# Optimization experiments

Hardware: AMD Instinct MI355X
Metric: run time of the kernel (lower is better)

Reference implementation:

```python
import jax, jax.numpy as jnp
import numpy as np

N, M = 30000, 32
VX, VY, VZ = 0.2, 0.2, 4.0
XOFF, YOFF, ZOFF = 0.1, -39.9, -1.0  # vx/2+pc_range[0], vy/2+pc_range[1], vz/2+pc_range[2]
EPS = 1e-3
H = 3  # num_heads, head_dim = 3 // 3 = 1


def setup_inputs() -> dict:
    key = jax.random.key(0)
    ks = jax.random.split(key, 13)
    features = jax.random.normal(ks[0], (N, M, 4), jnp.float32)
    num_points = jax.random.randint(ks[1], (N,), 1, M + 1, dtype=jnp.int32)
    coors = jax.random.randint(ks[2], (N, 4), 0, 352, dtype=jnp.int32)
    # PFN layer params (Linear 10->64 no bias, BN1d affine)
    pfn_w = jax.random.normal(ks[3], (10, 64), jnp.float32) * 0.1
    bn_gamma = jnp.ones((64,), jnp.float32)
    bn_beta = jnp.zeros((64,), jnp.float32)
    # PillarAttention: MHA on 3-dim coords, 3 heads of dim 1
    wq = jax.random.normal(ks[4], (3, 3), jnp.float32) * 0.5
    wk = jax.random.normal(ks[5], (3, 3), jnp.float32) * 0.5
    wv = jax.random.normal(ks[6], (3, 3), jnp.float32) * 0.5
    wo = jax.random.normal(ks[7], (3, 3), jnp.float32) * 0.5
    bq = jax.random.normal(ks[8], (3,), jnp.float32) * 0.02
    bk = jax.random.normal(ks[9], (3,), jnp.float32) * 0.02
    bv = jax.random.normal(ks[10], (3,), jnp.float32) * 0.02
    bo = jax.random.normal(ks[11], (3,), jnp.float32) * 0.02
    return dict(features=features, num_points=num_points, coors=coors,
                pfn_w=pfn_w, bn_gamma=bn_gamma, bn_beta=bn_beta,
                wq=wq, wk=wk, wv=wv, wo=wo, bq=bq, bk=bk, bv=bv, bo=bo)


def _pillar_attention(xyz, wq, wk, wv, wo, bq, bk, bv, bo):
    # xyz: (N, M, 3); 3 heads of dim 1 -> per-head score is an outer product
    q = xyz @ wq + bq  # (N, M, 3)
    k = xyz @ wk + bk
    v = xyz @ wv + bv
    # head_dim = 1 => scale = 1/sqrt(1) = 1
    scores = jnp.einsum('nih,njh->nhij', q, k)          # (N, H, M, M)
    attn = jax.nn.softmax(scores, axis=-1)
    out = jnp.einsum('nhij,njh->nih', attn, v)          # (N, M, 3)
    return out @ wo + bo


def reference(features, num_points, coors, pfn_w, bn_gamma, bn_beta,
              wq, wk, wv, wo, bq, bk, bv, bo):
    dtype = features.dtype
    xyz = features[:, :, :3]  # original coords (attn & cluster use these, pre in-place write)

    # PillarAttention on raw xyz, then max over feature dim
    feat_attn = _pillar_attention(xyz, wq, wk, wv, wo, bq, bk, bv, bo)  # (N, M, 3)
    max_attn = jnp.max(feat_attn, axis=-1, keepdims=True)              # (N, M, 1)

    npts = num_points.astype(dtype)[:, None, None]                      # (N,1,1)
    # cluster center offsets (uses original xyz)
    points_mean = jnp.sum(xyz, axis=1, keepdims=True) / npts
    f_cluster = xyz - points_mean                                       # (N, M, 3)

    # voxel center offsets; coors = [batch, z, y, x]
    cf = coors.astype(dtype)
    cx = cf[:, 3] * VX + XOFF
    cy = cf[:, 2] * VY + YOFF
    cz = cf[:, 1] * VZ + ZOFF
    f_center = jnp.stack([xyz[:, :, 0] - cx[:, None],
                          xyz[:, :, 1] - cy[:, None],
                          xyz[:, :, 2] - cz[:, None]], axis=-1)          # (N, M, 3)

    # legacy=True in-place bug: features[:, :, :3] becomes f_center before concat
    feats = jnp.concatenate([f_center, features[:, :, 3:], f_cluster, f_center], axis=-1)  # (N, M, 10)

    # mask out padded points
    mask = (jnp.arange(M)[None, :] < num_points[:, None]).astype(dtype)[:, :, None]
    feats = feats * mask

    # PFNLayer (last_vfe=True): Linear -> BN1d (train-mode stats over N*M) -> LeakyReLU
    x = feats @ pfn_w                                                    # (N, M, 64)
    mean = jnp.mean(x, axis=(0, 1))
    var = jnp.var(x, axis=(0, 1))
    x = (x - mean) * jax.lax.rsqrt(var + EPS) * bn_gamma + bn_beta
    x = jax.nn.leaky_relu(x, negative_slope=0.01)                        # (N, M, 64)

    # attention-weighted max pool fused with plain max pool
    fa = max_attn * x / jnp.sum(max_attn, axis=1, keepdims=True)
    fa = jnp.max(fa, axis=1, keepdims=True)                              # (N, 1, 64)
    fm = jnp.max(x, axis=1, keepdims=True)                               # (N, 1, 64)
    f = (fa + fm) * 0.5
    return f[:, 0, :]                                                    # (N, 64)
```

## Files before the change

### kernel.cpp

```cpp
#include <hip/hip_runtime.h>
#include <float.h>
#include <math.h>

constexpr int NP = 30000;
constexpr int M  = 32;
constexpr float VXc = 0.2f, VYc = 0.2f, VZc = 4.0f;
constexpr float XOFFc = 0.1f, YOFFc = -39.9f, ZOFFc = -1.0f;

typedef __attribute__((ext_vector_type(8)))  short bf16x8;
typedef __attribute__((ext_vector_type(16))) float f32x16;

__device__ __forceinline__ unsigned short f2bf(float x) {
    unsigned int u = __builtin_bit_cast(unsigned int, x);
    u = (u + 0x7fffu + ((u >> 16) & 1u)) >> 16;
    return (unsigned short)u;
}

__global__ __launch_bounds__(256) void stats_kernel(
    const float4* __restrict__ fp,
    const int*    __restrict__ num_points,
    const int*    __restrict__ coors,
    float*        __restrict__ Sp)
{
    float S[35];
#pragma unroll
    for (int k = 0; k < 35; ++k) S[k] = 0.f;

    const int stride = gridDim.x * blockDim.x;

    for (int p = blockIdx.x * blockDim.x + threadIdx.x; p < NP * M; p += stride) {
        const int n = p >> 5;
        const int i = p & 31;
        const float4 f = fp[p];

        float sx = f.x, sy = f.y, sz = f.z;
#pragma unroll
        for (int m = 16; m >= 1; m >>= 1) {
            sx += __shfl_xor(sx, m, 32);
            sy += __shfl_xor(sy, m, 32);
            sz += __shfl_xor(sz, m, 32);
        }
        const int npts = num_points[n];
        const float inv = __builtin_amdgcn_rcpf((float)npts);
        const int c1 = coors[4 * n + 1], c2 = coors[4 * n + 2], c3 = coors[4 * n + 3];
        const float cx = (float)c3 * VXc + XOFFc;
        const float cy = (float)c2 * VYc + YOFFc;
        const float cz = (float)c1 * VZc + ZOFFc;
        const bool valid = (i < npts);

        float u[7];
        u[0] = valid ? f.x - cx : 0.f;
        u[1] = valid ? f.y - cy : 0.f;
        u[2] = valid ? f.z - cz : 0.f;
        u[3] = valid ? f.w      : 0.f;
        u[4] = valid ? f.x - sx * inv : 0.f;
        u[5] = valid ? f.y - sy * inv : 0.f;
        u[6] = valid ? f.z - sz * inv : 0.f;

#pragma unroll
        for (int k = 0; k < 7; ++k) S[k] += u[k];
        int idx = 7;
#pragma unroll
        for (int k = 0; k < 7; ++k)
#pragma unroll
            for (int l = k; l < 7; ++l)
                S[idx++] += u[k] * u[l];
    }

#pragma unroll
    for (int k = 0; k < 35; ++k) {
#pragma unroll
        for (int m = 32; m >= 1; m >>= 1) S[k] += __shfl_xor(S[k], m, 64);
    }

    __shared__ float part[4][35];
    const int wid = threadIdx.x >> 6, ln = threadIdx.x & 63;
    if (ln == 0) {
#pragma unroll
        for (int k = 0; k < 35; ++k) part[wid][k] = S[k];
    }
    __syncthreads();
    if (threadIdx.x < 35) {
        Sp[blockIdx.x * 35 + threadIdx.x] =
            part[0][threadIdx.x] + part[1][threadIdx.x] +
            part[2][threadIdx.x] + part[3][threadIdx.x];
    }
}

__global__ __launch_bounds__(320) void affine_kernel(
    const float* __restrict__ Sp,
    int nsb,
    const float* __restrict__ pfn_w,
    const float* __restrict__ gamma,
    const float* __restrict__ beta,
    float*       __restrict__ AB,
    unsigned short* __restrict__ Wpk)
{
    __shared__ double sh[8][36];
    __shared__ double Sd[35];
    const int tid = threadIdx.x;

    if (tid < 280) {
        const int k = tid % 35;
        const int c = tid / 35;
        double acc = 0.0;
        for (int b = c; b < nsb; b += 8)
            acc += (double)Sp[b * 35 + k];
        sh[c][k] = acc;
    }
    __syncthreads();
    if (tid < 35) {
        double a = 0.0;
#pragma unroll
        for (int c = 0; c < 8; ++c) a += sh[c][tid];
        Sd[tid] = a;
    }
    __syncthreads();

    if (tid < 64) {
        const int c = tid;
        double w7[7];
        w7[0] = (double)pfn_w[0 * 64 + c] + (double)pfn_w[7 * 64 + c];
        w7[1] = (double)pfn_w[1 * 64 + c] + (double)pfn_w[8 * 64 + c];
        w7[2] = (double)pfn_w[2 * 64 + c] + (double)pfn_w[9 * 64 + c];
        w7[3] = (double)pfn_w[3 * 64 + c];
        w7[4] = (double)pfn_w[4 * 64 + c];
        w7[5] = (double)pfn_w[5 * 64 + c];
        w7[6] = (double)pfn_w[6 * 64 + c];

        const double invNM = 1.0 / ((double)NP * (double)M);
        double mean = 0.0;
#pragma unroll
        for (int k = 0; k < 7; ++k) mean += Sd[k] * w7[k];
        mean *= invNM;

        double ex2 = 0.0;
        int idx = 7;
#pragma unroll
        for (int k = 0; k < 7; ++k)
#pragma unroll
            for (int l = k; l < 7; ++l) {
                double t = Sd[idx++] * w7[k] * w7[l];
                ex2 += (k == l) ? t : 2.0 * t;
            }
        ex2 *= invNM;

        double var = ex2 - mean * mean;
        double a = (double)gamma[c] / sqrt(var + 1e-3);
        AB[c]      = (float)a;
        AB[64 + c] = (float)((double)beta[c] - mean * a);
    }

    if (tid < 256) {
        const int s = tid;
        const int v = s >> 7;
        const int t = (s >> 6) & 1;
        const int l = s & 63;
        const int half = l >> 5;
        const int n = (l & 31) + 32 * t;
        unsigned short val[8] = {0, 0, 0, 0, 0, 0, 0, 0};
        if (half == v) {
            float w7[7];
            w7[0] = pfn_w[0 * 64 + n] + pfn_w[7 * 64 + n];
            w7[1] = pfn_w[1 * 64 + n] + pfn_w[8 * 64 + n];
            w7[2] = pfn_w[2 * 64 + n] + pfn_w[9 * 64 + n];
            w7[3] = pfn_w[3 * 64 + n];
            w7[4] = pfn_w[4 * 64 + n];
            w7[5] = pfn_w[5 * 64 + n];
            w7[6] = pfn_w[6 * 64 + n];
#pragma unroll
            for (int j = 0; j < 7; ++j) val[j] = f2bf(w7[j]);
        }
#pragma unroll
        for (int j = 0; j < 8; ++j) Wpk[s * 8 + j] = val[j];
    }
}

__global__ __launch_bounds__(256) void main_kernel(
    const float4* __restrict__ fp,
    const int*    __restrict__ num_points,
    const int*    __restrict__ coors,
    const float*  __restrict__ AB,
    const unsigned short* __restrict__ Wpk,
    const float*  __restrict__ wq, const float* __restrict__ wk,
    const float*  __restrict__ wv, const float* __restrict__ wo,
    const float*  __restrict__ bq, const float* __restrict__ bk,
    const float*  __restrict__ bv, const float* __restrict__ bo,
    float*        __restrict__ out)
{
    const int tid  = threadIdx.x;
    const int wave = tid >> 6;
    const int lane = tid & 63;
    const int half = lane >> 5;
    const int i    = lane & 31;
    const int p    = wave * 2 + half;
    const int n    = blockIdx.x * 8 + p;

    __shared__ float kv_s[8][32][8];
    __shared__ float r_s[8][32];

    const float4 f = fp[(size_t)n * M + i];
    const int npts = num_points[n];
    const int c1 = coors[4 * n + 1], c2 = coors[4 * n + 2], c3 = coors[4 * n + 3];
    const float a_t0 = AB[i], a_t1 = AB[32 + i];
    const float b_t0 = AB[64 + i], b_t1 = AB[96 + i];
    const bf16x8 bfA0 = *reinterpret_cast<const bf16x8*>(Wpk + (size_t)(  0 + lane) * 8);
    const bf16x8 bfA1 = *reinterpret_cast<const bf16x8*>(Wpk + (size_t)( 64 + lane) * 8);
    const bf16x8 bfB0 = *reinterpret_cast<const bf16x8*>(Wpk + (size_t)(128 + lane) * 8);
    const bf16x8 bfB1 = *reinterpret_cast<const bf16x8*>(Wpk + (size_t)(192 + lane) * 8);

    float q[3], kk[3], vv[3];
#pragma unroll
    for (int h = 0; h < 3; ++h) {
        q[h]  = f.x * wq[0 * 3 + h] + f.y * wq[1 * 3 + h] + f.z * wq[2 * 3 + h] + bq[h];
        kk[h] = f.x * wk[0 * 3 + h] + f.y * wk[1 * 3 + h] + f.z * wk[2 * 3 + h] + bk[h];
        vv[h] = f.x * wv[0 * 3 + h] + f.y * wv[1 * 3 + h] + f.z * wv[2 * 3 + h] + bv[h];
    }
    *reinterpret_cast<float4*>(&kv_s[p][i][0]) = make_float4(kk[0], vv[0], kk[1], vv[1]);
    *reinterpret_cast<float2*>(&kv_s[p][i][4]) = make_float2(kk[2], vv[2]);

    float sx = f.x, sy = f.y, sz = f.z;
    float kmx[3], kmn[3];
#pragma unroll
    for (int h = 0; h < 3; ++h) { kmx[h] = kk[h]; kmn[h] = kk[h]; }
#pragma unroll
    for (int m = 16; m >= 1; m >>= 1) {
        sx += __shfl_xor(sx, m, 32);
        sy += __shfl_xor(sy, m, 32);
        sz += __shfl_xor(sz, m, 32);
#pragma unroll
        for (int h = 0; h < 3; ++h) {
            kmx[h] = fmaxf(kmx[h], __shfl_xor(kmx[h], m, 32));
            kmn[h] = fminf(kmn[h], __shfl_xor(kmn[h], m, 32));
        }
    }
    __syncthreads();

    const float LOG2E = 1.4426950408889634f;
    float qh2[3], mrow[3];
#pragma unroll
    for (int h = 0; h < 3; ++h) {
        qh2[h]  = q[h] * LOG2E;
        mrow[h] = qh2[h] * (q[h] >= 0.f ? kmx[h] : kmn[h]);
    }
    float den[3] = {0.f, 0.f, 0.f}, num[3] = {0.f, 0.f, 0.f};
#pragma unroll
    for (int j = 0; j < 32; ++j) {
        const float4 kv01 = *reinterpret_cast<const float4*>(&kv_s[p][j][0]);
        const float2 kv2  = *reinterpret_cast<const float2*>(&kv_s[p][j][4]);
        float e0 = __builtin_amdgcn_exp2f(__builtin_fmaf(qh2[0], kv01.x, -mrow[0]));
        float e1 = __builtin_amdgcn_exp2f(__builtin_fmaf(qh2[1], kv01.z, -mrow[1]));
        float e2 = __builtin_amdgcn_exp2f(__builtin_fmaf(qh2[2], kv2.x,  -mrow[2]));
        den[0] += e0; num[0] = __builtin_fmaf(e0, kv01.y, num[0]);
        den[1] += e1; num[1] = __builtin_fmaf(e1, kv01.w, num[1]);
        den[2] += e2; num[2] = __builtin_fmaf(e2, kv2.y,  num[2]);
    }
    const float o0 = num[0] * __builtin_amdgcn_rcpf(den[0]);
    const float o1 = num[1] * __builtin_amdgcn_rcpf(den[1]);
    const float o2 = num[2] * __builtin_amdgcn_rcpf(den[2]);

    float fa0 = o0 * wo[0] + o1 * wo[3] + o2 * wo[6] + bo[0];
    float fa1 = o0 * wo[1] + o1 * wo[4] + o2 * wo[7] + bo[1];
    float fa2 = o0 * wo[2] + o1 * wo[5] + o2 * wo[8] + bo[2];
    float ma  = fmaxf(fa0, fmaxf(fa1, fa2));

    float sum_ma = ma;
#pragma unroll
    for (int m = 16; m >= 1; m >>= 1) sum_ma += __shfl_xor(sum_ma, m, 32);
    r_s[p][i] = ma * __builtin_amdgcn_rcpf(sum_ma);

    const float inv = __builtin_amdgcn_rcpf((float)npts);
    const float cx = (float)c3 * VXc + XOFFc;
    const float cy = (float)c2 * VYc + YOFFc;
    const float cz = (float)c1 * VZc + ZOFFc;
    const bool valid = (i < npts);

    float u[7];
    u[0] = valid ? f.x - cx : 0.f;
    u[1] = valid ? f.y - cy : 0.f;
    u[2] = valid ? f.z - cz : 0.f;
    u[3] = valid ? f.w      : 0.f;
    u[4] = valid ? f.x - sx * inv : 0.f;
    u[5] = valid ? f.y - sy * inv : 0.f;
    u[6] = valid ? f.z - sz * inv : 0.f;

    unsigned int w32[4];
    w32[0] = (unsigned int)f2bf(u[0]) | ((unsigned int)f2bf(u[1]) << 16);
    w32[1] = (unsigned int)f2bf(u[2]) | ((unsigned int)f2bf(u[3]) << 16);
    w32[2] = (unsigned int)f2bf(u[4]) | ((unsigned int)f2bf(u[5]) << 16);
    w32[3] = (unsigned int)f2bf(u[6]);

    union { unsigned int w[4]; bf16x8 v; } ua, ub;
#pragma unroll
    for (int e = 0; e < 4; ++e) {
        ua.w[e] = (half == 0) ? w32[e] : 0u;
        ub.w[e] = (half == 1) ? w32[e] : 0u;
    }

    f32x16 accA0, accA1, accB0, accB1;
#pragma unroll
    for (int e = 0; e < 16; ++e) { accA0[e] = 0.f; accA1[e] = 0.f; accB0[e] = 0.f; accB1[e] = 0.f; }
    accA0 = __builtin_amdgcn_mfma_f32_32x32x16_bf16(ua.v, bfA0, accA0, 0, 0, 0);
    accA1 = __builtin_amdgcn_mfma_f32_32x32x16_bf16(ua.v, bfA1, accA1, 0, 0, 0);
    accB0 = __builtin_amdgcn_mfma_f32_32x32x16_bf16(ub.v, bfB0, accB0, 0, 0, 0);
    accB1 = __builtin_amdgcn_mfma_f32_32x32x16_bf16(ub.v, bfB1, accB1, 0, 0, 0);

    __syncthreads();

    const int pA = wave * 2;
    const int nA = blockIdx.x * 8 + pA;

    {
        float4 rg4[4];
#pragma unroll
        for (int g = 0; g < 4; ++g)
            rg4[g] = *reinterpret_cast<const float4*>(&r_s[pA][g * 8 + 4 * half]);

        float fm0 = -FLT_MAX, fv0 = -FLT_MAX, fm1 = -FLT_MAX, fv1 = -FLT_MAX;
#pragma unroll
        for (int rg = 0; rg < 16; ++rg) {
            const float rr = rg4[rg >> 2][rg & 3];
            float y0 = __builtin_fmaf(accA0[rg], a_t0, b_t0);
            y0 = fmaxf(y0, 0.01f * y0);
            fm0 = fmaxf(fm0, y0); fv0 = fmaxf(fv0, rr * y0);
            float y1 = __builtin_fmaf(accA1[rg], a_t1, b_t1);
            y1 = fmaxf(y1, 0.01f * y1);
            fm1 = fmaxf(fm1, y1); fv1 = fmaxf(fv1, rr * y1);
        }
        fm0 = fmaxf(fm0, __shfl_xor(fm0, 32, 64));
        fv0 = fmaxf(fv0, __shfl_xor(fv0, 32, 64));
        fm1 = fmaxf(fm1, __shfl_xor(fm1, 32, 64));
        fv1 = fmaxf(fv1, __shfl_xor(fv1, 32, 64));
        const float res = (half == 0) ? 0.5f * (fv0 + fm0) : 0.5f * (fv1 + fm1);
        out[(size_t)nA * 64 + 32 * half + i] = res;
    }

    {
        const int pB = pA + 1;
        const int nB = nA + 1;
        float4 rg4[4];
#pragma unroll
        for (int g = 0; g < 4; ++g)
            rg4[g] = *reinterpret_cast<const float4*>(&r_s[pB][g * 8 + 4 * half]);

        float fm0 = -FLT_MAX, fv0 = -FLT_MAX, fm1 = -FLT_MAX, fv1 = -FLT_MAX;
#pragma unroll
        for (int rg = 0; rg < 16; ++rg) {
            const float rr = rg4[rg >> 2][rg & 3];
            float y0 = __builtin_fmaf(accB0[rg], a_t0, b_t0);
            y0 = fmaxf(y0, 0.01f * y0);
            fm0 = fmaxf(fm0, y0); fv0 = fmaxf(fv0, rr * y0);
            float y1 = __builtin_fmaf(accB1[rg], a_t1, b_t1);
            y1 = fmaxf(y1, 0.01f * y1);
            fm1 = fmaxf(fm1, y1); fv1 = fmaxf(fv1, rr * y1);
        }
        fm0 = fmaxf(fm0, __shfl_xor(fm0, 32, 64));
        fv0 = fmaxf(fv0, __shfl_xor(fv0, 32, 64));
        fm1 = fmaxf(fm1, __shfl_xor(fm1, 32, 64));
        fv1 = fmaxf(fv1, __shfl_xor(fv1, 32, 64));
        const float res = (half == 0) ? 0.5f * (fv0 + fm0) : 0.5f * (fv1 + fm1);
        out[(size_t)nB * 64 + 32 * half + i] = res;
    }
}

extern "C" void kernel_launch(void* const* d_in, const int* in_sizes, int n_in,
                              void* d_out, int out_size, void* d_ws, size_t ws_size,
                              hipStream_t stream) {
    const float4* feats  = (const float4*)d_in[0];
    const int*    npts   = (const int*)d_in[1];
    const int*    coors  = (const int*)d_in[2];
    const float*  pfn_w  = (const float*)d_in[3];
    const float*  gamma  = (const float*)d_in[4];
    const float*  beta   = (const float*)d_in[5];
    const float*  wq     = (const float*)d_in[6];
    const float*  wk     = (const float*)d_in[7];
    const float*  wv     = (const float*)d_in[8];
    const float*  wo     = (const float*)d_in[9];
    const float*  bq     = (const float*)d_in[10];
    const float*  bk     = (const float*)d_in[11];
    const float*  bv     = (const float*)d_in[12];
    const float*  bo     = (const float*)d_in[13];
    float*        out    = (float*)d_out;

    int nsb = 480;
    if (ws_size > 0 && ws_size < (size_t)(480 * 140 + 8192)) {
        size_t avail = ws_size > 8192 ? ws_size - 8192 : 140;
        int fit = (int)(avail / 140);
        nsb = fit < 1 ? 1 : (fit > 480 ? 480 : fit);
    }
    size_t ab_off  = ((size_t)(nsb * 140) + 255) & ~(size_t)255;
    float*          Sp  = (float*)d_ws;
    float*          AB  = (float*)((char*)d_ws + ab_off);
    unsigned short* Wpk = (unsigned short*)((char*)d_ws + ab_off + 512);

    stats_kernel<<<nsb, 256, 0, stream>>>(feats, npts, coors, Sp);
    affine_kernel<<<1, 320, 0, stream>>>(Sp, nsb, pfn_w, gamma, beta, AB, Wpk);
    main_kernel<<<NP / 8, 256, 0, stream>>>(feats, npts, coors, AB, Wpk,
                                            wq, wk, wv, wo, bq, bk, bv, bo, out);
}
```

Measured before the change: 154.8 us.

## Fold BN affine into bf16 weights and run one-wave blocks with prefetch loop

The BatchNorm scale is folded into the packed bf16 PFN weights, and the shift rides along as an eighth weight row paired with a constant 1.0 input. That removes the per-element affine FMA and the AB loads in the main kernel. The main kernel now uses 64-thread blocks that loop over four pillar pairs, prefetching the next pair's inputs while computing the current one. The trade is more bf16 rounding on the scaled weights and bias, and less parallelism per block (3750 one-wave blocks).

```diff
diff --git a/kernel.cpp b/kernel.cpp
--- a/kernel.cpp
+++ b/kernel.cpp
@@ -93,11 +93,11 @@
     const float* __restrict__ pfn_w,
     const float* __restrict__ gamma,
     const float* __restrict__ beta,
-    float*       __restrict__ AB,
     unsigned short* __restrict__ Wpk)
 {
     __shared__ double sh[8][36];
     __shared__ double Sd[35];
+    __shared__ float a_sh[64], b_sh[64];
     const int tid = threadIdx.x;
 
     if (tid < 280) {
@@ -147,9 +147,10 @@
 
         double var = ex2 - mean * mean;
         double a = (double)gamma[c] / sqrt(var + 1e-3);
-        AB[c]      = (float)a;
-        AB[64 + c] = (float)((double)beta[c] - mean * a);
-    }
+        a_sh[c] = (float)a;
+        b_sh[c] = (float)((double)beta[c] - mean * a);
+    }
+    __syncthreads();
 
     if (tid < 256) {
         const int s = tid;
@@ -160,6 +161,7 @@
         const int n = (l & 31) + 32 * t;
         unsigned short val[8] = {0, 0, 0, 0, 0, 0, 0, 0};
         if (half == v) {
+            const float a = a_sh[n];
             float w7[7];
             w7[0] = pfn_w[0 * 64 + n] + pfn_w[7 * 64 + n];
             w7[1] = pfn_w[1 * 64 + n] + pfn_w[8 * 64 + n];
@@ -169,18 +171,18 @@
             w7[5] = pfn_w[5 * 64 + n];
             w7[6] = pfn_w[6 * 64 + n];
 #pragma unroll
-            for (int j = 0; j < 7; ++j) val[j] = f2bf(w7[j]);
+            for (int j = 0; j < 7; ++j) val[j] = f2bf(w7[j] * a);
+            val[7] = f2bf(b_sh[n]);
         }
 #pragma unroll
         for (int j = 0; j < 8; ++j) Wpk[s * 8 + j] = val[j];
     }
 }
 
-__global__ __launch_bounds__(256) void main_kernel(
+__global__ __launch_bounds__(64) void main_kernel(
     const float4* __restrict__ fp,
     const int*    __restrict__ num_points,
     const int*    __restrict__ coors,
-    const float*  __restrict__ AB,
     const unsigned short* __restrict__ Wpk,
     const float*  __restrict__ wq, const float* __restrict__ wk,
     const float*  __restrict__ wv, const float* __restrict__ wo,
@@ -188,178 +190,187 @@
     const float*  __restrict__ bv, const float* __restrict__ bo,
     float*        __restrict__ out)
 {
-    const int tid  = threadIdx.x;
-    const int wave = tid >> 6;
-    const int lane = tid & 63;
+    const int lane = threadIdx.x;
     const int half = lane >> 5;
     const int i    = lane & 31;
-    const int p    = wave * 2 + half;
-    const int n    = blockIdx.x * 8 + p;
-
-    __shared__ float kv_s[8][32][8];
-    __shared__ float r_s[8][32];
-
-    const float4 f = fp[(size_t)n * M + i];
-    const int npts = num_points[n];
-    const int c1 = coors[4 * n + 1], c2 = coors[4 * n + 2], c3 = coors[4 * n + 3];
-    const float a_t0 = AB[i], a_t1 = AB[32 + i];
-    const float b_t0 = AB[64 + i], b_t1 = AB[96 + i];
+
+    __shared__ float kv_s[2][32][8];
+    __shared__ float r_s[2][32];
+
     const bf16x8 bfA0 = *reinterpret_cast<const bf16x8*>(Wpk + (size_t)(  0 + lane) * 8);
     const bf16x8 bfA1 = *reinterpret_cast<const bf16x8*>(Wpk + (size_t)( 64 + lane) * 8);
     const bf16x8 bfB0 = *reinterpret_cast<const bf16x8*>(Wpk + (size_t)(128 + lane) * 8);
     const bf16x8 bfB1 = *reinterpret_cast<const bf16x8*>(Wpk + (size_t)(192 + lane) * 8);
 
-    float q[3], kk[3], vv[3];
-#pragma unroll
-    for (int h = 0; h < 3; ++h) {
-        q[h]  = f.x * wq[0 * 3 + h] + f.y * wq[1 * 3 + h] + f.z * wq[2 * 3 + h] + bq[h];
-        kk[h] = f.x * wk[0 * 3 + h] + f.y * wk[1 * 3 + h] + f.z * wk[2 * 3 + h] + bk[h];
-        vv[h] = f.x * wv[0 * 3 + h] + f.y * wv[1 * 3 + h] + f.z * wv[2 * 3 + h] + bv[h];
-    }
-    *reinterpret_cast<float4*>(&kv_s[p][i][0]) = make_float4(kk[0], vv[0], kk[1], vv[1]);
-    *reinterpret_cast<float2*>(&kv_s[p][i][4]) = make_float2(kk[2], vv[2]);
-
-    float sx = f.x, sy = f.y, sz = f.z;
-    float kmx[3], kmn[3];
-#pragma unroll
-    for (int h = 0; h < 3; ++h) { kmx[h] = kk[h]; kmn[h] = kk[h]; }
-#pragma unroll
-    for (int m = 16; m >= 1; m >>= 1) {
-        sx += __shfl_xor(sx, m, 32);
-        sy += __shfl_xor(sy, m, 32);
-        sz += __shfl_xor(sz, m, 32);
+    const int nbase = blockIdx.x * 8;
+
+    float4 f = fp[(size_t)(nbase + half) * M + i];
+    int np = num_points[nbase + half];
+    int c1 = coors[4 * (nbase + half) + 1];
+    int c2 = coors[4 * (nbase + half) + 2];
+    int c3 = coors[4 * (nbase + half) + 3];
+
+    const float LOG2E = 1.4426950408889634f;
+
+    for (int g = 0; g < 4; ++g) {
+        const int n = nbase + 2 * g + half;
+
+        float4 fn = f; int npn = np, c1n = c1, c2n = c2, c3n = c3;
+        if (g < 3) {
+            const int nn = n + 2;
+            fn  = fp[(size_t)nn * M + i];
+            npn = num_points[nn];
+            c1n = coors[4 * nn + 1];
+            c2n = coors[4 * nn + 2];
+            c3n = coors[4 * nn + 3];
+        }
+
+        float q[3], kk[3], vv[3];
 #pragma unroll
         for (int h = 0; h < 3; ++h) {
-            kmx[h] = fmaxf(kmx[h], __shfl_xor(kmx[h], m, 32));
-            kmn[h] = fminf(kmn[h], __shfl_xor(kmn[h], m, 32));
-        }
-    }
-    __syncthreads();
-
-    const float LOG2E = 1.4426950408889634f;
-    float qh2[3], mrow[3];
-#pragma unroll
-    for (int h = 0; h < 3; ++h) {
-        qh2[h]  = q[h] * LOG2E;
-        mrow[h] = qh2[h] * (q[h] >= 0.f ? kmx[h] : kmn[h]);
-    }
-    float den[3] = {0.f, 0.f, 0.f}, num[3] = {0.f, 0.f, 0.f};
-#pragma unroll
-    for (int j = 0; j < 32; ++j) {
-        const float4 kv01 = *reinterpret_cast<const float4*>(&kv_s[p][j][0]);
-        const float2 kv2  = *reinterpret_cast<const float2*>(&kv_s[p][j][4]);
-        float e0 = __builtin_amdgcn_exp2f(__builtin_fmaf(qh2[0], kv01.x, -mrow[0]));
-        float e1 = __builtin_amdgcn_exp2f(__builtin_fmaf(qh2[1], kv01.z, -mrow[1]));
-        float e2 = __builtin_amdgcn_exp2f(__builtin_fmaf(qh2[2], kv2.x,  -mrow[2]));
-        den[0] += e0; num[0] = __builtin_fmaf(e0, kv01.y, num[0]);
-        den[1] += e1; num[1] = __builtin_fmaf(e1, kv01.w, num[1]);
-        den[2] += e2; num[2] = __builtin_fmaf(e2, kv2.y,  num[2]);
-    }
-    const float o0 = num[0] * __builtin_amdgcn_rcpf(den[0]);
-    const float o1 = num[1] * __builtin_amdgcn_rcpf(den[1]);
-    const float o2 = num[2] * __builtin_amdgcn_rcpf(den[2]);
-
-    float fa0 = o0 * wo[0] + o1 * wo[3] + o2 * wo[6] + bo[0];
-    float fa1 = o0 * wo[1] + o1 * wo[4] + o2 * wo[7] + bo[1];
-    float fa2 = o0 * wo[2] + o1 * wo[5] + o2 * wo[8] + bo[2];
-    float ma  = fmaxf(fa0, fmaxf(fa1, fa2));
-
-    float sum_ma = ma;
-#pragma unroll
-    for (int m = 16; m >= 1; m >>= 1) sum_ma += __shfl_xor(sum_ma, m, 32);
-    r_s[p][i] = ma * __builtin_amdgcn_rcpf(sum_ma);
-
-    const float inv = __builtin_amdgcn_rcpf((float)npts);
-    const float cx = (float)c3 * VXc + XOFFc;
-    const float cy = (float)c2 * VYc + YOFFc;
-    const float cz = (float)c1 * VZc + ZOFFc;
-    const bool valid = (i < npts);
-
-    float u[7];
-    u[0] = valid ? f.x - cx : 0.f;
-    u[1] = valid ? f.y - cy : 0.f;
-    u[2] = valid ? f.z - cz : 0.f;
-    u[3] = valid ? f.w      : 0.f;
-    u[4] = valid ? f.x - sx * inv : 0.f;
-    u[5] = valid ? f.y - sy * inv : 0.f;
-    u[6] = valid ? f.z - sz * inv : 0.f;
-
-    unsigned int w32[4];
-    w32[0] = (unsigned int)f2bf(u[0]) | ((unsigned int)f2bf(u[1]) << 16);
-    w32[1] = (unsigned int)f2bf(u[2]) | ((unsigned int)f2bf(u[3]) << 16);
-    w32[2] = (unsigned int)f2bf(u[4]) | ((unsigned int)f2bf(u[5]) << 16);
-    w32[3] = (unsigned int)f2bf(u[6]);
-
-    union { unsigned int w[4]; bf16x8 v; } ua, ub;
-#pragma unroll
-    for (int e = 0; e < 4; ++e) {
-        ua.w[e] = (half == 0) ? w32[e] : 0u;
-        ub.w[e] = (half == 1) ? w32[e] : 0u;
-    }
-
-    f32x16 accA0, accA1, accB0, accB1;
-#pragma unroll
-    for (int e = 0; e < 16; ++e) { accA0[e] = 0.f; accA1[e] = 0.f; accB0[e] = 0.f; accB1[e] = 0.f; }
-    accA0 = __builtin_amdgcn_mfma_f32_32x32x16_bf16(ua.v, bfA0, accA0, 0, 0, 0);
-    accA1 = __builtin_amdgcn_mfma_f32_32x32x16_bf16(ua.v, bfA1, accA1, 0, 0, 0);
-    accB0 = __builtin_amdgcn_mfma_f32_32x32x16_bf16(ub.v, bfB0, accB0, 0, 0, 0);
-    accB1 = __builtin_amdgcn_mfma_f32_32x32x16_bf16(ub.v, bfB1, accB1, 0, 0, 0);
-
-    __syncthreads();
-
-    const int pA = wave * 2;
-    const int nA = blockIdx.x * 8 + pA;
-
-    {
-        float4 rg4[4];
-#pragma unroll
-        for (int g = 0; g < 4; ++g)
-            rg4[g] = *reinterpret_cast<const float4*>(&r_s[pA][g * 8 + 4 * half]);
-
-        float fm0 = -FLT_MAX, fv0 = -FLT_MAX, fm1 = -FLT_MAX, fv1 = -FLT_MAX;
-#pragma unroll
-        for (int rg = 0; rg < 16; ++rg) {
-            const float rr = rg4[rg >> 2][rg & 3];
-            float y0 = __builtin_fmaf(accA0[rg], a_t0, b_t0);
-            y0 = fmaxf(y0, 0.01f * y0);
-            fm0 = fmaxf(fm0, y0); fv0 = fmaxf(fv0, rr * y0);
-            float y1 = __builtin_fmaf(accA1[rg], a_t1, b_t1);
-            y1 = fmaxf(y1, 0.01f * y1);
-            fm1 = fmaxf(fm1, y1); fv1 = fmaxf(fv1, rr * y1);
-        }
-        fm0 = fmaxf(fm0, __shfl_xor(fm0, 32, 64));
-        fv0 = fmaxf(fv0, __shfl_xor(fv0, 32, 64));
-        fm1 = fmaxf(fm1, __shfl_xor(fm1, 32, 64));
-        fv1 = fmaxf(fv1, __shfl_xor(fv1, 32, 64));
-        const float res = (half == 0) ? 0.5f * (fv0 + fm0) : 0.5f * (fv1 + fm1);
-        out[(size_t)nA * 64 + 32 * half + i] = res;
-    }
-
-    {
-        const int pB = pA + 1;
-        const int nB = nA + 1;
-        float4 rg4[4];
-#pragma unroll
-        for (int g = 0; g < 4; ++g)
-            rg4[g] = *reinterpret_cast<const float4*>(&r_s[pB][g * 8 + 4 * half]);
-
-        float fm0 = -FLT_MAX, fv0 = -FLT_MAX, fm1 = -FLT_MAX, fv1 = -FLT_MAX;
-#pragma unroll
-        for (int rg = 0; rg < 16; ++rg) {
-            const float rr = rg4[rg >> 2][rg & 3];
-            float y0 = __builtin_fmaf(accB0[rg], a_t0, b_t0);
-            y0 = fmaxf(y0, 0.01f * y0);
-            fm0 = fmaxf(fm0, y0); fv0 = fmaxf(fv0, rr * y0);
-            float y1 = __builtin_fmaf(accB1[rg], a_t1, b_t1);
-            y1 = fmaxf(y1, 0.01f * y1);
-            fm1 = fmaxf(fm1, y1); fv1 = fmaxf(fv1, rr * y1);
-        }
-        fm0 = fmaxf(fm0, __shfl_xor(fm0, 32, 64));
-        fv0 = fmaxf(fv0, __shfl_xor(fv0, 32, 64));
-        fm1 = fmaxf(fm1, __shfl_xor(fm1, 32, 64));
-        fv1 = fmaxf(fv1, __shfl_xor(fv1, 32, 64));
-        const float res = (half == 0) ? 0.5f * (fv0 + fm0) : 0.5f * (fv1 + fm1);
-        out[(size_t)nB * 64 + 32 * half + i] = res;
+            q[h]  = f.x * wq[0 * 3 + h] + f.y * wq[1 * 3 + h] + f.z * wq[2 * 3 + h] + bq[h];
+            kk[h] = f.x * wk[0 * 3 + h] + f.y * wk[1 * 3 + h] + f.z * wk[2 * 3 + h] + bk[h];
+            vv[h] = f.x * wv[0 * 3 + h] + f.y * wv[1 * 3 + h] + f.z * wv[2 * 3 + h] + bv[h];
+        }
+        *reinterpret_cast<float4*>(&kv_s[half][i][0]) = make_float4(kk[0], vv[0], kk[1], vv[1]);
+        *reinterpret_cast<float2*>(&kv_s[half][i][4]) = make_float2(kk[2], vv[2]);
+
+        float sx = f.x, sy = f.y, sz = f.z;
+        float kmx[3], kmn[3];
+#pragma unroll
+        for (int h = 0; h < 3; ++h) { kmx[h] = kk[h]; kmn[h] = kk[h]; }
+#pragma unroll
+        for (int m = 16; m >= 1; m >>= 1) {
+            sx += __shfl_xor(sx, m, 32);
+            sy += __shfl_xor(sy, m, 32);
+            sz += __shfl_xor(sz, m, 32);
+#pragma unroll
+            for (int h = 0; h < 3; ++h) {
+                kmx[h] = fmaxf(kmx[h], __shfl_xor(kmx[h], m, 32));
+                kmn[h] = fminf(kmn[h], __shfl_xor(kmn[h], m, 32));
+            }
+        }
+        __syncthreads();
+
+        float qh2[3], mrow[3];
+#pragma unroll
+        for (int h = 0; h < 3; ++h) {
+            qh2[h]  = q[h] * LOG2E;
+            mrow[h] = qh2[h] * (q[h] >= 0.f ? kmx[h] : kmn[h]);
+        }
+        float den[3] = {0.f, 0.f, 0.f}, num[3] = {0.f, 0.f, 0.f};
+#pragma unroll
+        for (int j = 0; j < 32; ++j) {
+            const float4 kv01 = *reinterpret_cast<const float4*>(&kv_s[half][j][0]);
+            const float2 kv2  = *reinterpret_cast<const float2*>(&kv_s[half][j][4]);
+            float e0 = __builtin_amdgcn_exp2f(__builtin_fmaf(qh2[0], kv01.x, -mrow[0]));
+            float e1 = __builtin_amdgcn_exp2f(__builtin_fmaf(qh2[1], kv01.z, -mrow[1]));
+            float e2 = __builtin_amdgcn_exp2f(__builtin_fmaf(qh2[2], kv2.x,  -mrow[2]));
+            den[0] += e0; num[0] = __builtin_fmaf(e0, kv01.y, num[0]);
+            den[1] += e1; num[1] = __builtin_fmaf(e1, kv01.w, num[1]);
+            den[2] += e2; num[2] = __builtin_fmaf(e2, kv2.y,  num[2]);
+        }
+        const float o0 = num[0] * __builtin_amdgcn_rcpf(den[0]);
+        const float o1 = num[1] * __builtin_amdgcn_rcpf(den[1]);
+        const float o2 = num[2] * __builtin_amdgcn_rcpf(den[2]);
+
+        float fa0 = o0 * wo[0] + o1 * wo[3] + o2 * wo[6] + bo[0];
+        float fa1 = o0 * wo[1] + o1 * wo[4] + o2 * wo[7] + bo[1];
+        float fa2 = o0 * wo[2] + o1 * wo[5] + o2 * wo[8] + bo[2];
+        float ma  = fmaxf(fa0, fmaxf(fa1, fa2));
+
+        float sum_ma = ma;
+#pragma unroll
+        for (int m = 16; m >= 1; m >>= 1) sum_ma += __shfl_xor(sum_ma, m, 32);
+        r_s[half][i] = ma * __builtin_amdgcn_rcpf(sum_ma);
+
+        const float inv = __builtin_amdgcn_rcpf((float)np);
+        const float cx = (float)c3 * VXc + XOFFc;
+        const float cy = (float)c2 * VYc + YOFFc;
+        const float cz = (float)c1 * VZc + ZOFFc;
+        const bool valid = (i < np);
+
+        float u[7];
+        u[0] = valid ? f.x - cx : 0.f;
+        u[1] = valid ? f.y - cy : 0.f;
+        u[2] = valid ? f.z - cz : 0.f;
+        u[3] = valid ? f.w      : 0.f;
+        u[4] = valid ? f.x - sx * inv : 0.f;
+        u[5] = valid ? f.y - sy * inv : 0.f;
+        u[6] = valid ? f.z - sz * inv : 0.f;
+
+        unsigned int w32[4];
+        w32[0] = (unsigned int)f2bf(u[0]) | ((unsigned int)f2bf(u[1]) << 16);
+        w32[1] = (unsigned int)f2bf(u[2]) | ((unsigned int)f2bf(u[3]) << 16);
+        w32[2] = (unsigned int)f2bf(u[4]) | ((unsigned int)f2bf(u[5]) << 16);
+        w32[3] = (unsigned int)f2bf(u[6]) | (0x3F80u << 16);
+
+        union { unsigned int w[4]; bf16x8 v; } ua, ub;
+#pragma unroll
+        for (int e = 0; e < 4; ++e) {
+            ua.w[e] = (half == 0) ? w32[e] : 0u;
+            ub.w[e] = (half == 1) ? w32[e] : 0u;
+        }
+
+        f32x16 accA0 = {}, accA1 = {}, accB0 = {}, accB1 = {};
+        accA0 = __builtin_amdgcn_mfma_f32_32x32x16_bf16(ua.v, bfA0, accA0, 0, 0, 0);
+        accA1 = __builtin_amdgcn_mfma_f32_32x32x16_bf16(ua.v, bfA1, accA1, 0, 0, 0);
+        accB0 = __builtin_amdgcn_mfma_f32_32x32x16_bf16(ub.v, bfB0, accB0, 0, 0, 0);
+        accB1 = __builtin_amdgcn_mfma_f32_32x32x16_bf16(ub.v, bfB1, accB1, 0, 0, 0);
+
+        __syncthreads();
+
+        {
+            float4 rg4[4];
+#pragma unroll
+            for (int gg = 0; gg < 4; ++gg)
+                rg4[gg] = *reinterpret_cast<const float4*>(&r_s[0][gg * 8 + 4 * half]);
+
+            float fm0 = -FLT_MAX, fv0 = -FLT_MAX, fm1 = -FLT_MAX, fv1 = -FLT_MAX;
+#pragma unroll
+            for (int rg = 0; rg < 16; ++rg) {
+                const float rr = rg4[rg >> 2][rg & 3];
+                float y0 = accA0[rg];
+                y0 = fmaxf(y0, 0.01f * y0);
+                fm0 = fmaxf(fm0, y0); fv0 = fmaxf(fv0, rr * y0);
+                float y1 = accA1[rg];
+                y1 = fmaxf(y1, 0.01f * y1);
+                fm1 = fmaxf(fm1, y1); fv1 = fmaxf(fv1, rr * y1);
+            }
+            fm0 = fmaxf(fm0, __shfl_xor(fm0, 32, 64));
+            fv0 = fmaxf(fv0, __shfl_xor(fv0, 32, 64));
+            fm1 = fmaxf(fm1, __shfl_xor(fm1, 32, 64));
+            fv1 = fmaxf(fv1, __shfl_xor(fv1, 32, 64));
+            const float res = (half == 0) ? 0.5f * (fv0 + fm0) : 0.5f * (fv1 + fm1);
+            out[(size_t)(nbase + 2 * g) * 64 + 32 * half + i] = res;
+        }
+
+        {
+            float4 rg4[4];
+#pragma unroll
+            for (int gg = 0; gg < 4; ++gg)
+                rg4[gg] = *reinterpret_cast<const float4*>(&r_s[1][gg * 8 + 4 * half]);
+
+            float fm0 = -FLT_MAX, fv0 = -FLT_MAX, fm1 = -FLT_MAX, fv1 = -FLT_MAX;
+#pragma unroll
+            for (int rg = 0; rg < 16; ++rg) {
+                const float rr = rg4[rg >> 2][rg & 3];
+                float y0 = accB0[rg];
+                y0 = fmaxf(y0, 0.01f * y0);
+                fm0 = fmaxf(fm0, y0); fv0 = fmaxf(fv0, rr * y0);
+                float y1 = accB1[rg];
+                y1 = fmaxf(y1, 0.01f * y1);
+                fm1 = fmaxf(fm1, y1); fv1 = fmaxf(fv1, rr * y1);
+            }
+            fm0 = fmaxf(fm0, __shfl_xor(fm0, 32, 64));
+            fv0 = fmaxf(fv0, __shfl_xor(fv0, 32, 64));
+            fm1 = fmaxf(fm1, __shfl_xor(fm1, 32, 64));
+            fv1 = fmaxf(fv1, __shfl_xor(fv1, 32, 64));
+            const float res = (half == 0) ? 0.5f * (fv0 + fm0) : 0.5f * (fv1 + fm1);
+            out[(size_t)(nbase + 2 * g + 1) * 64 + 32 * half + i] = res;
+        }
+
+        f = fn; np = npn; c1 = c1n; c2 = c2n; c3 = c3n;
     }
 }
 
@@ -388,13 +399,12 @@
         int fit = (int)(avail / 140);
         nsb = fit < 1 ? 1 : (fit > 480 ? 480 : fit);
     }
-    size_t ab_off  = ((size_t)(nsb * 140) + 255) & ~(size_t)255;
+    size_t wpk_off = ((size_t)(nsb * 140) + 255) & ~(size_t)255;
     float*          Sp  = (float*)d_ws;
-    float*          AB  = (float*)((char*)d_ws + ab_off);
-    unsigned short* Wpk = (unsigned short*)((char*)d_ws + ab_off + 512);
+    unsigned short* Wpk = (unsigned short*)((char*)d_ws + wpk_off);
 
     stats_kernel<<<nsb, 256, 0, stream>>>(feats, npts, coors, Sp);
-    affine_kernel<<<1, 320, 0, stream>>>(Sp, nsb, pfn_w, gamma, beta, AB, Wpk);
-    main_kernel<<<NP / 8, 256, 0, stream>>>(feats, npts, coors, AB, Wpk,
-                                            wq, wk, wv, wo, bq, bk, bv, bo, out);
+    affine_kernel<<<1, 320, 0, stream>>>(Sp, nsb, pfn_w, gamma, beta, Wpk);
+    main_kernel<<<NP / 8, 64, 0, stream>>>(feats, npts, coors, Wpk,
+                                           wq, wk, wv, wo, bq, bk, bv, bo, out);
 }
```

Result: no change. 154.4 us (-0.2%).
